# Kernel tuning notes

Measured on AMD Instinct MI355X. Metric: run time of the kernel, lower is better.

Reference implementation:

```python
import jax, jax.numpy as jnp
import numpy as np

B, L, ENC, DEC, HID = 256, 196, 2048, 512, 512


def setup_inputs() -> dict:
    key = jax.random.key(0)
    ks = jax.random.split(key, 8)
    s_enc = 1.0 / np.sqrt(ENC)
    s_dec = 1.0 / np.sqrt(DEC)
    s_hid = 1.0 / np.sqrt(HID)
    return {
        "feature": jax.random.normal(ks[0], (B, L, ENC), dtype=jnp.float32),
        "hidden": jax.random.normal(ks[1], (B, DEC), dtype=jnp.float32),
        # nn.Linear params (PyTorch default uniform init ranges)
        "Wf": jax.random.uniform(ks[2], (HID, ENC), jnp.float32, -s_enc, s_enc),
        "bf": jax.random.uniform(ks[3], (HID,), jnp.float32, -s_enc, s_enc),
        "Wh": jax.random.uniform(ks[4], (HID, DEC), jnp.float32, -s_dec, s_dec),
        "bh": jax.random.uniform(ks[5], (HID,), jnp.float32, -s_dec, s_dec),
        "We": jax.random.uniform(ks[6], (1, HID), jnp.float32, -s_hid, s_hid),
        "be": jax.random.uniform(ks[7], (1,), jnp.float32, -s_hid, s_hid),
    }


def reference(feature, hidden, Wf, bf, Wh, bh, We, be):
    # feature: [B, L, ENC], hidden: [B, DEC]
    feat_emb = jnp.einsum("ble,he->blh", feature, Wf) + bf          # [B, L, HID]
    hid_emb = (hidden @ Wh.T + bh)[:, None, :]                        # [B, 1, HID]
    emb = jax.nn.relu(feat_emb + hid_emb)                             # [B, L, HID]
    score = jnp.einsum("blh,h->bl", emb, We[0]) + be[0]               # [B, L]
    weight = jax.nn.softmax(score, axis=1)                            # [B, L]
    output = jnp.einsum("bl,ble->be", weight, feature)                # [B, ENC]
    return (output, weight)
```

## Files before the change

### kernel.cpp

```cpp
#include <hip/hip_runtime.h>
#include <hip/hip_bf16.h>
#include <math.h>

#define B_   256
#define L_   196
#define ENC_ 2048
#define DEC_ 512
#define HID_ 512

typedef __attribute__((ext_vector_type(8))) short short8v;
typedef __attribute__((ext_vector_type(4))) short short4v;
typedef __attribute__((ext_vector_type(4))) float f32x4;

static __device__ __forceinline__ short f2bf(float x) {
    unsigned u = __float_as_uint(x);
    u += 0x7fffu + ((u >> 16) & 1u);
    return (short)(u >> 16);
}

__global__ __launch_bounds__(256) void kconvert(const float* __restrict__ Wf,
                                                short* __restrict__ wfbf) {
    int idx = (blockIdx.x * 256 + threadIdx.x) * 4;
    int n  = idx >> 11;
    int e0 = idx & 2047;
    float4 f = *(const float4*)(Wf + idx);
    short4v h;
    h.x = f2bf(f.x); h.y = f2bf(f.y); h.z = f2bf(f.z); h.w = f2bf(f.w);
    int tile = e0 >> 5;
    int lu   = (e0 >> 3) & 3;
    int pu   = lu ^ ((n >> 1) & 3);
    int off  = n * 2048 + tile * 32 + pu * 8 + (e0 & 7);
    *(short4v*)(wfbf + off) = h;
}

__global__ __launch_bounds__(512) void khid(const float* __restrict__ hidden,
                                            const float* __restrict__ Wh,
                                            const float* __restrict__ bh,
                                            float* __restrict__ hid_emb) {
    __shared__ float hs[8][512];
    int t = threadIdx.x;
    int bg = blockIdx.x * 8;
    #pragma unroll
    for (int i = 0; i < 8; ++i) hs[i][t] = hidden[(size_t)(bg + i) * 512 + t];
    __syncthreads();
    float acc[8] = {0.f,0.f,0.f,0.f,0.f,0.f,0.f,0.f};
    const float4* wrow = (const float4*)(Wh + (size_t)t * 512);
    #pragma unroll 4
    for (int d4 = 0; d4 < 128; ++d4) {
        float4 w = wrow[d4];
        int d = d4 * 4;
        #pragma unroll
        for (int i = 0; i < 8; ++i)
            acc[i] += w.x * hs[i][d] + w.y * hs[i][d+1] + w.z * hs[i][d+2] + w.w * hs[i][d+3];
    }
    float bhv = bh[t];
    #pragma unroll
    for (int i = 0; i < 8; ++i)
        hid_emb[(size_t)(bg + i) * 512 + t] = acc[i] + bhv;
}

__global__ __launch_bounds__(512, 4) void kscore(
    const float* __restrict__ feat, const short* __restrict__ wfbf,
    const float* __restrict__ bf, const float* __restrict__ hid_emb,
    const float* __restrict__ We, const float* __restrict__ be,
    float* __restrict__ score)
{
    __shared__ short lds_b[2 * 512 * 32];
    __shared__ short lds_a[2 * 64 * 32];
    __shared__ float score_s[8][64];

    const int tid  = threadIdx.x;
    const int wave = tid >> 6;
    const int lane = tid & 63;
    const int g    = lane >> 4;
    const int c    = lane & 15;
    const int m0   = blockIdx.x * 64;

    const int r_a  = tid >> 3;
    const int c4   = tid & 7;
    const float* gA = feat + (size_t)(m0 + r_a) * ENC_ + c4 * 4;
    const int boffA = r_a * 64 + (((c4 >> 1) ^ ((r_a >> 1) & 3)) << 4) + (c4 & 1) * 8;

    f32x4 acc[4][4];
    #pragma unroll
    for (int i = 0; i < 4; ++i)
        #pragma unroll
        for (int j = 0; j < 4; ++j)
            acc[i][j] = (f32x4)0.f;

#define STAGE_B(K0, BUF)                                                      \
    {                                                                         \
        short* bbase = lds_b + (size_t)(BUF) * 16384;                         \
        _Pragma("unroll")                                                     \
        for (int j = 0; j < 4; ++j) {                                         \
            int ubase = j * 512 + wave * 64;       \
            int ulin  = ubase + lane;              \
            int n = ulin >> 2, u = ulin & 3;                                  \
            const short* gp = wfbf + (size_t)n * ENC_ + (K0) + u * 8;         \
            short* lp = bbase + (size_t)ubase * 8;                            \
            __builtin_amdgcn_global_load_lds(                                 \
                (const __attribute__((address_space(1))) void*)gp,            \
                (__attribute__((address_space(3))) void*)lp, 16, 0, 0);       \
        }                                                                     \
    }

#define COMPUTE_TILE(BUF)                                                     \
    {                                                                         \
        const char* la = (const char*)lds_a + (BUF) * 4096;                   \
        const char* lb = (const char*)lds_b + (BUF) * 32768;                  \
        short8v af[4], bq[4];                                                 \
        _Pragma("unroll")                                                     \
        for (int mi = 0; mi < 4; ++mi) {                                      \
            int row = mi * 16 + c;                                            \
            int un  = g ^ ((row >> 1) & 3);                                   \
            af[mi] = *(const short8v*)(la + row * 64 + un * 16);              \
        }                                                                     \
        _Pragma("unroll")                                                     \
        for (int ni = 0; ni < 4; ++ni) {                                      \
            int n  = wave * 64 + ni * 16 + c;                                 \
            int un = g ^ ((n >> 1) & 3);                                      \
            bq[ni] = *(const short8v*)(lb + n * 64 + un * 16);                \
        }                                                                     \
        _Pragma("unroll")                                                     \
        for (int mi = 0; mi < 4; ++mi)                                        \
            _Pragma("unroll")                                                 \
            for (int ni = 0; ni < 4; ++ni)                                    \
                acc[mi][ni] = __builtin_amdgcn_mfma_f32_16x16x32_bf16(        \
                    af[mi], bq[ni], acc[mi][ni], 0, 0, 0);                    \
    }

#define WRITE_A(FA, BUF)                                                      \
    {                                                                         \
        short4v h0;                                                           \
        h0.x = f2bf((FA).x); h0.y = f2bf((FA).y);                             \
        h0.z = f2bf((FA).z); h0.w = f2bf((FA).w);                             \
        char* wa = (char*)lds_a + (BUF) * 4096;                               \
        *(short4v*)(wa + boffA) = h0;                                         \
    }

#define BAR_COUNTED(N)                                                        \
    asm volatile("s_waitcnt vmcnt(" #N ") lgkmcnt(0)" ::: "memory");          \
    __builtin_amdgcn_sched_barrier(0);                                        \
    __builtin_amdgcn_s_barrier();                                             \
    __builtin_amdgcn_sched_barrier(0);

    float4 fa_cur = *(const float4*)(gA);
    STAGE_B(0, 0)
    float4 fa_nxt = *(const float4*)(gA + 32);
    WRITE_A(fa_cur, 0)
    fa_cur = fa_nxt;
    BAR_COUNTED(1)

    for (int kt = 0; kt < 62; ++kt) {
        const int pcur = kt & 1;
        STAGE_B((kt + 1) * 32, pcur ^ 1)
        fa_nxt = *(const float4*)(gA + (kt + 2) * 32);
        COMPUTE_TILE(pcur)
        WRITE_A(fa_cur, pcur ^ 1)
        fa_cur = fa_nxt;
        BAR_COUNTED(1)
    }
    STAGE_B(63 * 32, 1)
    COMPUTE_TILE(0)
    WRITE_A(fa_cur, 1)
    BAR_COUNTED(0)
    COMPUTE_TILE(1)

#undef STAGE_B
#undef COMPUTE_TILE
#undef WRITE_A
#undef BAR_COUNTED

    float wev[4], bfv[4];
    #pragma unroll
    for (int ni = 0; ni < 4; ++ni) {
        int n = wave * 64 + ni * 16 + c;
        wev[ni] = We[n];
        bfv[ni] = bf[n];
    }
    #pragma unroll
    for (int mi = 0; mi < 4; ++mi) {
        float part[4] = {0.f, 0.f, 0.f, 0.f};
        #pragma unroll
        for (int j = 0; j < 4; ++j) {
            int row  = mi * 16 + g * 4 + j;
            int bidx = (m0 + row) / 196;
            const float* hrow = hid_emb + (size_t)bidx * 512;
            #pragma unroll
            for (int ni = 0; ni < 4; ++ni) {
                int n = wave * 64 + ni * 16 + c;
                float v = acc[mi][ni][j] + bfv[ni] + hrow[n];
                v = fmaxf(v, 0.f);
                part[j] += v * wev[ni];
            }
        }
        #pragma unroll
        for (int j = 0; j < 4; ++j) {
            float p = part[j];
            p += __shfl_xor(p, 1, 16);
            p += __shfl_xor(p, 2, 16);
            p += __shfl_xor(p, 4, 16);
            p += __shfl_xor(p, 8, 16);
            if (c == 0) score_s[wave][mi * 16 + g * 4 + j] = p;
        }
    }
    __syncthreads();
    if (tid < 64) {
        float s = be[0];
        #pragma unroll
        for (int w = 0; w < 8; ++w) s += score_s[w][tid];
        score[m0 + tid] = s;
    }
}

__global__ __launch_bounds__(256) void kout(
    const float* __restrict__ score, const float* __restrict__ feat,
    float* __restrict__ out_o, float* __restrict__ out_w)
{
    __shared__ float wbuf[196];
    __shared__ float red[8];
    int t    = threadIdx.x;
    int b    = blockIdx.x >> 1;
    int half = blockIdx.x & 1;
    int w    = t >> 6, lane = t & 63;

    float s = (t < 196) ? score[b * 196 + t] : -1e30f;
    float m = s;
    #pragma unroll
    for (int off = 32; off >= 1; off >>= 1) m = fmaxf(m, __shfl_xor(m, off, 64));
    if (lane == 0) red[w] = m;
    __syncthreads();
    m = fmaxf(fmaxf(red[0], red[1]), fmaxf(red[2], red[3]));
    float e = (t < 196) ? __expf(s - m) : 0.f;
    float sum = e;
    #pragma unroll
    for (int off = 32; off >= 1; off >>= 1) sum += __shfl_xor(sum, off, 64);
    if (lane == 0) red[4 + w] = sum;
    __syncthreads();
    sum = red[4] + red[5] + red[6] + red[7];
    float wt = e / sum;
    if (t < 196) {
        wbuf[t] = wt;
        if (half == 0) out_w[b * 196 + t] = wt;
    }
    __syncthreads();

    int e0 = half * 1024 + t * 4;
    float4 acc = make_float4(0.f, 0.f, 0.f, 0.f);
    const float* fb = feat + (size_t)b * L_ * ENC_ + e0;
    #pragma unroll 4
    for (int l = 0; l < 196; ++l) {
        float4 v = *(const float4*)(fb + (size_t)l * ENC_);
        float wl = wbuf[l];
        acc.x += wl * v.x; acc.y += wl * v.y; acc.z += wl * v.z; acc.w += wl * v.w;
    }
    *(float4*)(out_o + (size_t)b * ENC_ + e0) = acc;
}

extern "C" void kernel_launch(void* const* d_in, const int* in_sizes, int n_in,
                              void* d_out, int out_size, void* d_ws, size_t ws_size,
                              hipStream_t stream) {
    (void)in_sizes; (void)n_in; (void)out_size; (void)ws_size;
    const float* feature = (const float*)d_in[0];
    const float* hidden  = (const float*)d_in[1];
    const float* Wf      = (const float*)d_in[2];
    const float* bf      = (const float*)d_in[3];
    const float* Wh      = (const float*)d_in[4];
    const float* bh      = (const float*)d_in[5];
    const float* We      = (const float*)d_in[6];
    const float* be      = (const float*)d_in[7];

    char* ws = (char*)d_ws;
    short* wfbf    = (short*)ws;
    float* hid_emb = (float*)(ws + (2u << 20));
    float* score   = (float*)(ws + (2u << 20) + (512u << 10));

    float* out_o = (float*)d_out;
    float* out_w = out_o + (size_t)B_ * ENC_;

    kconvert<<<dim3(1024), dim3(256), 0, stream>>>(Wf, wfbf);
    khid<<<dim3(32), dim3(512), 0, stream>>>(hidden, Wh, bh, hid_emb);
    kscore<<<dim3(784), dim3(512), 0, stream>>>(feature, wfbf, bf, hid_emb, We, be, score);
    kout<<<dim3(512), dim3(256), 0, stream>>>(score, feature, (float*)d_out, out_w);
}
```

Measured before the change: 318.8 us.

## Load Wf bf16 fragments directly into registers instead of staging through LDS

Drops the swizzled LDS staging of the bf16 weight tile (global_load_lds plus LDS reads). Each lane now loads its B fragments straight from global memory into registers, double-buffered across iterations, and kconvert writes a plain row-major layout. This removes 64KB of LDS per block and the vmcnt waits at the barriers, which may raise occupancy. The cost is that every block re-reads the full weight matrix from L2 through uncoalesced 16-byte per-lane loads, exposing global latency inside the MFMA loop.

New measurement: 399.2 us. 1.25x slower.

```diff
diff --git a/kernel.cpp b/kernel.cpp
--- a/kernel.cpp
+++ b/kernel.cpp
@@ -21,16 +21,10 @@
 __global__ __launch_bounds__(256) void kconvert(const float* __restrict__ Wf,
                                                 short* __restrict__ wfbf) {
     int idx = (blockIdx.x * 256 + threadIdx.x) * 4;
-    int n  = idx >> 11;
-    int e0 = idx & 2047;
     float4 f = *(const float4*)(Wf + idx);
     short4v h;
     h.x = f2bf(f.x); h.y = f2bf(f.y); h.z = f2bf(f.z); h.w = f2bf(f.w);
-    int tile = e0 >> 5;
-    int lu   = (e0 >> 3) & 3;
-    int pu   = lu ^ ((n >> 1) & 3);
-    int off  = n * 2048 + tile * 32 + pu * 8 + (e0 & 7);
-    *(short4v*)(wfbf + off) = h;
+    *(short4v*)(wfbf + idx) = h;
 }
 
 __global__ __launch_bounds__(512) void khid(const float* __restrict__ hidden,
@@ -65,7 +59,6 @@
     const float* __restrict__ We, const float* __restrict__ be,
     float* __restrict__ score)
 {
-    __shared__ short lds_b[2 * 512 * 32];
     __shared__ short lds_a[2 * 64 * 32];
     __shared__ float score_s[8][64];
 
@@ -81,6 +74,9 @@
     const float* gA = feat + (size_t)(m0 + r_a) * ENC_ + c4 * 4;
     const int boffA = r_a * 64 + (((c4 >> 1) ^ ((r_a >> 1) & 3)) << 4) + (c4 & 1) * 8;
 
+    const char* gB = (const char*)wfbf
+                   + ((size_t)(wave * 64 + c) * ENC_ + g * 8) * 2;
+
     f32x4 acc[4][4];
     #pragma unroll
     for (int i = 0; i < 4; ++i)
@@ -88,45 +84,26 @@
         for (int j = 0; j < 4; ++j)
             acc[i][j] = (f32x4)0.f;
 
-#define STAGE_B(K0, BUF)                                                      \
-    {                                                                         \
-        short* bbase = lds_b + (size_t)(BUF) * 16384;                         \
-        _Pragma("unroll")                                                     \
-        for (int j = 0; j < 4; ++j) {                                         \
-            int ubase = j * 512 + wave * 64;       \
-            int ulin  = ubase + lane;              \
-            int n = ulin >> 2, u = ulin & 3;                                  \
-            const short* gp = wfbf + (size_t)n * ENC_ + (K0) + u * 8;         \
-            short* lp = bbase + (size_t)ubase * 8;                            \
-            __builtin_amdgcn_global_load_lds(                                 \
-                (const __attribute__((address_space(1))) void*)gp,            \
-                (__attribute__((address_space(3))) void*)lp, 16, 0, 0);       \
-        }                                                                     \
-    }
-
-#define COMPUTE_TILE(BUF)                                                     \
+    short8v bqA[4], bqB[4];
+
+#define LOAD_BQ(DST, KT)                                                      \
+    _Pragma("unroll")                                                         \
+    for (int ni = 0; ni < 4; ++ni)                                            \
+        DST[ni] = *(const short8v*)(gB + ni * 65536 + (KT) * 64);
+
+#define COMPUTE(BQ, BUF)                                                      \
     {                                                                         \
         const char* la = (const char*)lds_a + (BUF) * 4096;                   \
-        const char* lb = (const char*)lds_b + (BUF) * 32768;                  \
-        short8v af[4], bq[4];                                                 \
         _Pragma("unroll")                                                     \
         for (int mi = 0; mi < 4; ++mi) {                                      \
             int row = mi * 16 + c;                                            \
             int un  = g ^ ((row >> 1) & 3);                                   \
-            af[mi] = *(const short8v*)(la + row * 64 + un * 16);              \
-        }                                                                     \
-        _Pragma("unroll")                                                     \
-        for (int ni = 0; ni < 4; ++ni) {                                      \
-            int n  = wave * 64 + ni * 16 + c;                                 \
-            int un = g ^ ((n >> 1) & 3);                                      \
-            bq[ni] = *(const short8v*)(lb + n * 64 + un * 16);                \
-        }                                                                     \
-        _Pragma("unroll")                                                     \
-        for (int mi = 0; mi < 4; ++mi)                                        \
+            short8v af = *(const short8v*)(la + row * 64 + un * 16);          \
             _Pragma("unroll")                                                 \
             for (int ni = 0; ni < 4; ++ni)                                    \
                 acc[mi][ni] = __builtin_amdgcn_mfma_f32_16x16x32_bf16(        \
-                    af[mi], bq[ni], acc[mi][ni], 0, 0, 0);                    \
+                    af, BQ[ni], acc[mi][ni], 0, 0, 0);                        \
+        }                                                                     \
     }
 
 #define WRITE_A(FA, BUF)                                                      \
@@ -138,38 +115,42 @@
         *(short4v*)(wa + boffA) = h0;                                         \
     }
 
-#define BAR_COUNTED(N)                                                        \
-    asm volatile("s_waitcnt vmcnt(" #N ") lgkmcnt(0)" ::: "memory");          \
+#define LBAR                                                                  \
+    asm volatile("s_waitcnt lgkmcnt(0)" ::: "memory");                        \
     __builtin_amdgcn_sched_barrier(0);                                        \
     __builtin_amdgcn_s_barrier();                                             \
     __builtin_amdgcn_sched_barrier(0);
 
+#define ITER(KT, CUR, NXT)                                                    \
+    {                                                                         \
+        const int ka = ((KT) + 2 <= 63) ? (KT) + 2 : 63;           \
+        fa_nxt = *(const float4*)(gA + ka * 32);                  \
+        LOAD_BQ(NXT, (KT) + 1)                                    \
+        COMPUTE(CUR, (KT) & 1)                                                \
+        WRITE_A(fa_cur, ((KT) & 1) ^ 1)                           \
+        fa_cur = fa_nxt;                                                      \
+        LBAR                                                                  \
+    }
+
     float4 fa_cur = *(const float4*)(gA);
-    STAGE_B(0, 0)
     float4 fa_nxt = *(const float4*)(gA + 32);
+    LOAD_BQ(bqA, 0)
     WRITE_A(fa_cur, 0)
     fa_cur = fa_nxt;
-    BAR_COUNTED(1)
-
-    for (int kt = 0; kt < 62; ++kt) {
-        const int pcur = kt & 1;
-        STAGE_B((kt + 1) * 32, pcur ^ 1)
-        fa_nxt = *(const float4*)(gA + (kt + 2) * 32);
-        COMPUTE_TILE(pcur)
-        WRITE_A(fa_cur, pcur ^ 1)
-        fa_cur = fa_nxt;
-        BAR_COUNTED(1)
-    }
-    STAGE_B(63 * 32, 1)
-    COMPUTE_TILE(0)
-    WRITE_A(fa_cur, 1)
-    BAR_COUNTED(0)
-    COMPUTE_TILE(1)
-
-#undef STAGE_B
-#undef COMPUTE_TILE
+    LBAR
+
+    for (int kt2 = 0; kt2 < 31; ++kt2) {
+        ITER(2 * kt2,     bqA, bqB)
+        ITER(2 * kt2 + 1, bqB, bqA)
+    }
+    ITER(62, bqA, bqB)
+    COMPUTE(bqB, 1)
+
+#undef LOAD_BQ
+#undef COMPUTE
 #undef WRITE_A
-#undef BAR_COUNTED
+#undef LBAR
+#undef ITER
 
     float wev[4], bfv[4];
     #pragma unroll
```

## Deepen kscore pipeline to triple-buffered B tiles and longer A prefetch

Applied to the files above, without the earlier changes.

Changes the GEMM main loop in kscore from double-buffered to triple-buffered LDS staging of the bf16 weight tiles, with the A (feature) global loads prefetched several K-steps ahead through a register queue. The wait count at each barrier is relaxed so two B stages can be in flight while computing. The aim is to hide global memory latency better. The extra LDS and registers force the occupancy hint down from 4 to 2 blocks per CU, which may reduce latency hiding across blocks.

After: 395.8 us. 24.2% more time.

```diff
diff --git a/kernel.cpp b/kernel.cpp
--- a/kernel.cpp
+++ b/kernel.cpp
@@ -59,13 +59,13 @@
         hid_emb[(size_t)(bg + i) * 512 + t] = acc[i] + bhv;
 }
 
-__global__ __launch_bounds__(512, 4) void kscore(
+__global__ __launch_bounds__(512, 2) void kscore(
     const float* __restrict__ feat, const short* __restrict__ wfbf,
     const float* __restrict__ bf, const float* __restrict__ hid_emb,
     const float* __restrict__ We, const float* __restrict__ be,
     float* __restrict__ score)
 {
-    __shared__ short lds_b[2 * 512 * 32];
+    __shared__ short lds_b[3 * 512 * 32];
     __shared__ short lds_a[2 * 64 * 32];
     __shared__ float score_s[8][64];
 
@@ -104,10 +104,10 @@
         }                                                                     \
     }
 
-#define COMPUTE_TILE(BUF)                                                     \
+#define COMPUTE_TILE(ABUF, BBUF)                                              \
     {                                                                         \
-        const char* la = (const char*)lds_a + (BUF) * 4096;                   \
-        const char* lb = (const char*)lds_b + (BUF) * 32768;                  \
+        const char* la = (const char*)lds_a + (ABUF) * 4096;                  \
+        const char* lb = (const char*)lds_b + (size_t)(BBUF) * 32768;         \
         short8v af[4], bq[4];                                                 \
         _Pragma("unroll")                                                     \
         for (int mi = 0; mi < 4; ++mi) {                                      \
@@ -144,27 +144,33 @@
     __builtin_amdgcn_s_barrier();                                             \
     __builtin_amdgcn_sched_barrier(0);
 
-    float4 fa_cur = *(const float4*)(gA);
+    float4 a0  = *(const float4*)(gA);
     STAGE_B(0, 0)
-    float4 fa_nxt = *(const float4*)(gA + 32);
-    WRITE_A(fa_cur, 0)
-    fa_cur = fa_nxt;
-    BAR_COUNTED(1)
-
+    STAGE_B(32, 1)
+    float4 fa0 = *(const float4*)(gA + 32);
+    float4 fa1 = *(const float4*)(gA + 64);
+    float4 fa2 = *(const float4*)(gA + 96);
+    float4 fa3;
+    WRITE_A(a0, 0)
+    BAR_COUNTED(7)
+
+    int bc = 0;
+    int bs = 2;
     for (int kt = 0; kt < 62; ++kt) {
-        const int pcur = kt & 1;
-        STAGE_B((kt + 1) * 32, pcur ^ 1)
-        fa_nxt = *(const float4*)(gA + (kt + 2) * 32);
-        COMPUTE_TILE(pcur)
-        WRITE_A(fa_cur, pcur ^ 1)
-        fa_cur = fa_nxt;
-        BAR_COUNTED(1)
-    }
-    STAGE_B(63 * 32, 1)
-    COMPUTE_TILE(0)
-    WRITE_A(fa_cur, 1)
+        STAGE_B((kt + 2) * 32, bs)
+        int ka = (kt + 4 > 63) ? 63 : kt + 4;
+        fa3 = *(const float4*)(gA + ka * 32);
+        COMPUTE_TILE(kt & 1, bc)
+        WRITE_A(fa0, (kt & 1) ^ 1)
+        fa0 = fa1; fa1 = fa2; fa2 = fa3;
+        BAR_COUNTED(6)
+        bc = (bc == 2) ? 0 : bc + 1;
+        bs = (bs == 2) ? 0 : bs + 1;
+    }
+    COMPUTE_TILE(0, 2)
+    WRITE_A(fa0, 1)
     BAR_COUNTED(0)
-    COMPUTE_TILE(1)
+    COMPUTE_TILE(1, 0)
 
 #undef STAGE_B
 #undef COMPUTE_TILE
```

## Load feature A-fragments directly into registers and retile waves as 2x4

Applied to the files above, without the earlier changes.

The score kernel no longer stages the feature tile in LDS. Each wave loads its own rows from global memory straight into the MFMA operand layout and converts them to bf16 in registers. The wave grid changes from 8 waves sharing all 64 rows to a 2x4 arrangement of 32 rows by 128 columns, and the epilogue reduction is adjusted to match. This removes the LDS writes and reads for A and their bank traffic. In exchange, each feature row is fetched by four waves, which raises L1/L2 request traffic, and each wave now reads twice as many B fragments from LDS.

Result: slower. 469.2 us (+47.2%).

```diff
diff --git a/kernel.cpp b/kernel.cpp
--- a/kernel.cpp
+++ b/kernel.cpp
@@ -66,35 +66,37 @@
     float* __restrict__ score)
 {
     __shared__ short lds_b[2 * 512 * 32];
-    __shared__ short lds_a[2 * 64 * 32];
-    __shared__ float score_s[8][64];
+    __shared__ float score_s[8][32];
 
     const int tid  = threadIdx.x;
     const int wave = tid >> 6;
     const int lane = tid & 63;
     const int g    = lane >> 4;
     const int c    = lane & 15;
+    const int wr   = wave >> 2;
+    const int wc   = wave & 3;
     const int m0   = blockIdx.x * 64;
 
-    const int r_a  = tid >> 3;
-    const int c4   = tid & 7;
-    const float* gA = feat + (size_t)(m0 + r_a) * ENC_ + c4 * 4;
-    const int boffA = r_a * 64 + (((c4 >> 1) ^ ((r_a >> 1) & 3)) << 4) + (c4 & 1) * 8;
-
-    f32x4 acc[4][4];
-    #pragma unroll
-    for (int i = 0; i < 4; ++i)
-        #pragma unroll
-        for (int j = 0; j < 4; ++j)
+    const float* gA0 = feat + (size_t)(m0 + wr * 32 + c) * ENC_ + g * 8;
+    const float* gA1 = gA0 + (size_t)16 * ENC_;
+
+    f32x4 acc[2][8];
+    #pragma unroll
+    for (int i = 0; i < 2; ++i)
+        #pragma unroll
+        for (int j = 0; j < 8; ++j)
             acc[i][j] = (f32x4)0.f;
+
+    short8v af0, af1;
+    float4 a00, a01, a10, a11;
 
 #define STAGE_B(K0, BUF)                                                      \
     {                                                                         \
         short* bbase = lds_b + (size_t)(BUF) * 16384;                         \
         _Pragma("unroll")                                                     \
         for (int j = 0; j < 4; ++j) {                                         \
-            int ubase = j * 512 + wave * 64;       \
-            int ulin  = ubase + lane;              \
+            int ubase = j * 512 + wave * 64;           \
+            int ulin  = ubase + lane;                  \
             int n = ulin >> 2, u = ulin & 3;                                  \
             const short* gp = wfbf + (size_t)n * ENC_ + (K0) + u * 8;         \
             short* lp = bbase + (size_t)ubase * 8;                            \
@@ -104,38 +106,46 @@
         }                                                                     \
     }
 
+#define LOAD_A(KT)                                                            \
+    {                                                                         \
+        const float* p0 = gA0 + (KT) * 32;                                    \
+        const float* p1 = gA1 + (KT) * 32;                                    \
+        a00 = *(const float4*)(p0);  a01 = *(const float4*)(p0 + 4);          \
+        a10 = *(const float4*)(p1);  a11 = *(const float4*)(p1 + 4);          \
+    }
+
+#define CONV_A                                                                \
+    {                                                                         \
+        short8v t0, t1;                                                       \
+        t0[0]=f2bf(a00.x); t0[1]=f2bf(a00.y); t0[2]=f2bf(a00.z);              \
+        t0[3]=f2bf(a00.w); t0[4]=f2bf(a01.x); t0[5]=f2bf(a01.y);              \
+        t0[6]=f2bf(a01.z); t0[7]=f2bf(a01.w);                                 \
+        t1[0]=f2bf(a10.x); t1[1]=f2bf(a10.y); t1[2]=f2bf(a10.z);              \
+        t1[3]=f2bf(a10.w); t1[4]=f2bf(a11.x); t1[5]=f2bf(a11.y);              \
+        t1[6]=f2bf(a11.z); t1[7]=f2bf(a11.w);                                 \
+        af0 = t0; af1 = t1;                                                   \
+    }
+
 #define COMPUTE_TILE(BUF)                                                     \
     {                                                                         \
-        const char* la = (const char*)lds_a + (BUF) * 4096;                   \
-        const char* lb = (const char*)lds_b + (BUF) * 32768;                  \
-        short8v af[4], bq[4];                                                 \
+        const char* lb = (const char*)lds_b + (size_t)(BUF) * 32768;          \
         _Pragma("unroll")                                                     \
-        for (int mi = 0; mi < 4; ++mi) {                                      \
-            int row = mi * 16 + c;                                            \
-            int un  = g ^ ((row >> 1) & 3);                                   \
-            af[mi] = *(const short8v*)(la + row * 64 + un * 16);              \
+        for (int nh = 0; nh < 2; ++nh) {                                      \
+            short8v bq[4];                                                    \
+            _Pragma("unroll")                                                 \
+            for (int ni = 0; ni < 4; ++ni) {                                  \
+                int n  = wc * 128 + nh * 64 + ni * 16 + c;                    \
+                int un = g ^ ((n >> 1) & 3);                                  \
+                bq[ni] = *(const short8v*)(lb + n * 64 + un * 16);            \
+            }                                                                 \
+            _Pragma("unroll")                                                 \
+            for (int ni = 0; ni < 4; ++ni) {                                  \
+                acc[0][nh*4+ni] = __builtin_amdgcn_mfma_f32_16x16x32_bf16(    \
+                    af0, bq[ni], acc[0][nh*4+ni], 0, 0, 0);                   \
+                acc[1][nh*4+ni] = __builtin_amdgcn_mfma_f32_16x16x32_bf16(    \
+                    af1, bq[ni], acc[1][nh*4+ni], 0, 0, 0);                   \
+            }                                                                 \
         }                                                                     \
-        _Pragma("unroll")                                                     \
-        for (int ni = 0; ni < 4; ++ni) {                                      \
-            int n  = wave * 64 + ni * 16 + c;                                 \
-            int un = g ^ ((n >> 1) & 3);                                      \
-            bq[ni] = *(const short8v*)(lb + n * 64 + un * 16);                \
-        }                                                                     \
-        _Pragma("unroll")                                                     \
-        for (int mi = 0; mi < 4; ++mi)                                        \
-            _Pragma("unroll")                                                 \
-            for (int ni = 0; ni < 4; ++ni)                                    \
-                acc[mi][ni] = __builtin_amdgcn_mfma_f32_16x16x32_bf16(        \
-                    af[mi], bq[ni], acc[mi][ni], 0, 0, 0);                    \
-    }
-
-#define WRITE_A(FA, BUF)                                                      \
-    {                                                                         \
-        short4v h0;                                                           \
-        h0.x = f2bf((FA).x); h0.y = f2bf((FA).y);                             \
-        h0.z = f2bf((FA).z); h0.w = f2bf((FA).w);                             \
-        char* wa = (char*)lds_a + (BUF) * 4096;                               \
-        *(short4v*)(wa + boffA) = h0;                                         \
     }
 
 #define BAR_COUNTED(N)                                                        \
@@ -144,54 +154,52 @@
     __builtin_amdgcn_s_barrier();                                             \
     __builtin_amdgcn_sched_barrier(0);
 
-    float4 fa_cur = *(const float4*)(gA);
+    LOAD_A(0)
     STAGE_B(0, 0)
-    float4 fa_nxt = *(const float4*)(gA + 32);
-    WRITE_A(fa_cur, 0)
-    fa_cur = fa_nxt;
-    BAR_COUNTED(1)
-
-    for (int kt = 0; kt < 62; ++kt) {
-        const int pcur = kt & 1;
-        STAGE_B((kt + 1) * 32, pcur ^ 1)
-        fa_nxt = *(const float4*)(gA + (kt + 2) * 32);
-        COMPUTE_TILE(pcur)
-        WRITE_A(fa_cur, pcur ^ 1)
-        fa_cur = fa_nxt;
-        BAR_COUNTED(1)
-    }
-    STAGE_B(63 * 32, 1)
-    COMPUTE_TILE(0)
-    WRITE_A(fa_cur, 1)
-    BAR_COUNTED(0)
+    CONV_A
+    LOAD_A(1)
+    BAR_COUNTED(4)
+
+    for (int kt = 0; kt < 63; ++kt) {
+        const int buf = kt & 1;
+        STAGE_B((kt + 1) * 32, buf ^ 1)
+        COMPUTE_TILE(buf)
+        CONV_A
+        {
+            const int ka = (kt + 2 > 63) ? 63 : kt + 2;
+            LOAD_A(ka)
+        }
+        BAR_COUNTED(4)
+    }
     COMPUTE_TILE(1)
 
 #undef STAGE_B
+#undef LOAD_A
+#undef CONV_A
 #undef COMPUTE_TILE
-#undef WRITE_A
 #undef BAR_COUNTED
 
-    float wev[4], bfv[4];
-    #pragma unroll
-    for (int ni = 0; ni < 4; ++ni) {
-        int n = wave * 64 + ni * 16 + c;
-        wev[ni] = We[n];
-        bfv[ni] = bf[n];
-    }
-    #pragma unroll
-    for (int mi = 0; mi < 4; ++mi) {
+    float wev[8], bfv[8];
+    #pragma unroll
+    for (int q = 0; q < 8; ++q) {
+        int n = wc * 128 + (q >> 2) * 64 + (q & 3) * 16 + c;
+        wev[q] = We[n];
+        bfv[q] = bf[n];
+    }
+    #pragma unroll
+    for (int mi = 0; mi < 2; ++mi) {
         float part[4] = {0.f, 0.f, 0.f, 0.f};
         #pragma unroll
         for (int j = 0; j < 4; ++j) {
-            int row  = mi * 16 + g * 4 + j;
-            int bidx = (m0 + row) / 196;
+            int row  = m0 + wr * 32 + mi * 16 + g * 4 + j;
+            int bidx = row / 196;
             const float* hrow = hid_emb + (size_t)bidx * 512;
             #pragma unroll
-            for (int ni = 0; ni < 4; ++ni) {
-                int n = wave * 64 + ni * 16 + c;
-                float v = acc[mi][ni][j] + bfv[ni] + hrow[n];
+            for (int q = 0; q < 8; ++q) {
+                int n = wc * 128 + (q >> 2) * 64 + (q & 3) * 16 + c;
+                float v = acc[mi][q][j] + bfv[q] + hrow[n];
                 v = fmaxf(v, 0.f);
-                part[j] += v * wev[ni];
+                part[j] += v * wev[q];
             }
         }
         #pragma unroll
@@ -206,10 +214,12 @@
     }
     __syncthreads();
     if (tid < 64) {
+        int r   = tid;
+        int wrr = r >> 5;
         float s = be[0];
         #pragma unroll
-        for (int w = 0; w < 8; ++w) s += score_s[w][tid];
-        score[m0 + tid] = s;
+        for (int wcc = 0; wcc < 4; ++wcc) s += score_s[wrr * 4 + wcc][r & 31];
+        score[m0 + r] = s;
     }
 }
 
```
